# Optimization experiments

Hardware: AMD Instinct MI355X
Metric: run time of the kernel (lower is better)

## Reference

```python
import jax, jax.numpy as jnp
import numpy as np

B, IN_DIM, OUT_DIM, N = 8, 128, 128, 256
BN_EPS = 1e-5


def setup_inputs() -> dict:
    key = jax.random.key(0)
    ks = jax.random.split(key, 6)
    A = jax.random.normal(ks[0], (B, IN_DIM, N), dtype=jnp.float32)
    ini_p = float(np.sqrt(3.0 / OUT_DIM / IN_DIM))
    ini_qk = float(np.sqrt(1.0 / OUT_DIM / IN_DIM))
    P1 = jax.random.uniform(ks[1], (OUT_DIM, IN_DIM), minval=-ini_p, maxval=ini_p, dtype=jnp.float32)
    P2 = jax.random.uniform(ks[2], (OUT_DIM, IN_DIM), minval=-ini_p, maxval=ini_p, dtype=jnp.float32)
    q = jax.random.uniform(ks[3], (OUT_DIM, IN_DIM), minval=-ini_qk, maxval=ini_qk, dtype=jnp.float32)
    k = jax.random.uniform(ks[4], (OUT_DIM, IN_DIM), minval=-ini_qk, maxval=ini_qk, dtype=jnp.float32)
    gamma = jnp.ones((OUT_DIM,), dtype=jnp.float32)
    beta = jnp.zeros((OUT_DIM,), dtype=jnp.float32)
    return {"A": A, "P1": P1, "P2": P2, "q": q, "k": k,
            "gamma": gamma, "beta": beta,
            "permutation_size1": N, "BATCH_SIZE": B}


def reference(A, P1, P2, q, k, gamma, beta, permutation_size1, BATCH_SIZE):
    # A: [B, in_dim, n]; params [out_dim, in_dim]
    A1 = jnp.einsum('oi,bin->bon', P1, A)            # [B, C, n]
    Q = jnp.einsum('oi,bin->bon', q, A)              # [B, C, n]
    K = jnp.einsum('oi,bin->bon', k, A)              # [B, C, n]
    # Rank-1 outer product per (b, c): Alpha[b,c,i,j] = Q[b,c,i] * K[b,c,j]
    Alpha = Q[..., :, None] * K[..., None, :]        # [B, C, n, n]
    row_norm = jnp.linalg.norm(Alpha, axis=3, keepdims=True)  # [B, C, n, 1]
    Alpha_norm = jnp.abs(Alpha) / row_norm
    V = jnp.einsum('oi,bin->bon', P2, A)             # [B, C, n]
    Y = jnp.einsum('bcij,bcj->bci', Alpha_norm, V)   # [B, C, n]
    out = A1 + V + 0.1 * Y
    out = jax.nn.relu(out)
    # BatchNorm1d (training mode): normalize per channel over (B, n)
    mean = out.mean(axis=(0, 2), keepdims=True)
    var = out.var(axis=(0, 2), keepdims=True)
    out = (out - mean) * jax.lax.rsqrt(var + BN_EPS)
    out = out * gamma[None, :, None] + beta[None, :, None]
    return out
```

## Files before the change

### kernel.cpp

```cpp
#include <hip/hip_runtime.h>
#include <math.h>

#define BB   8
#define IND  128
#define OUTD 128
#define NN   256
#define NQ   64
#define BN_EPS 1e-5f

__global__ __launch_bounds__(64) void k1_proj(
    const float* __restrict__ A,
    const float* __restrict__ P1,
    const float* __restrict__ P2,
    const float* __restrict__ kw,
    float* __restrict__ pbuf,
    float* __restrict__ bnp)
{
    const int c = blockIdx.x;
    const int b = blockIdx.y;
    const int x = threadIdx.x;

    const float4* __restrict__ A4 = (const float4*)A + (size_t)b * IND * NQ;
    const float* __restrict__ w1 = P1 + c * IND;
    const float* __restrict__ w2 = P2 + c * IND;
    const float* __restrict__ w3 = kw + c * IND;

    float a1[4] = {0.f, 0.f, 0.f, 0.f};
    float vv[4] = {0.f, 0.f, 0.f, 0.f};
    float kv[4] = {0.f, 0.f, 0.f, 0.f};

    #pragma unroll
    for (int blk = 0; blk < 16; ++blk) {
        float4 cur[8];
        #pragma unroll
        for (int j = 0; j < 8; ++j)
            cur[j] = A4[(blk * 8 + j) * NQ + x];
        #pragma unroll
        for (int j = 0; j < 8; ++j) {
            const int i = blk * 8 + j;
            const float wa = w1[i], wb = w2[i], wc = w3[i];
            a1[0] = fmaf(wa, cur[j].x, a1[0]); a1[1] = fmaf(wa, cur[j].y, a1[1]);
            a1[2] = fmaf(wa, cur[j].z, a1[2]); a1[3] = fmaf(wa, cur[j].w, a1[3]);
            vv[0] = fmaf(wb, cur[j].x, vv[0]); vv[1] = fmaf(wb, cur[j].y, vv[1]);
            vv[2] = fmaf(wb, cur[j].z, vv[2]); vv[3] = fmaf(wb, cur[j].w, vv[3]);
            kv[0] = fmaf(wc, cur[j].x, kv[0]); kv[1] = fmaf(wc, cur[j].y, kv[1]);
            kv[2] = fmaf(wc, cur[j].z, kv[2]); kv[3] = fmaf(wc, cur[j].w, kv[3]);
        }
    }

    float s2 = 0.f, sv = 0.f;
    #pragma unroll
    for (int j = 0; j < 4; ++j) {
        s2 = fmaf(kv[j], kv[j], s2);
        sv = fmaf(fabsf(kv[j]), vv[j], sv);
    }
    #pragma unroll
    for (int off = 32; off >= 1; off >>= 1) {
        s2 += __shfl_xor(s2, off, 64);
        sv += __shfl_xor(sv, off, 64);
    }
    const float y = sv / sqrtf(s2);

    float p[4];
    float bnsum = 0.f, bnsq = 0.f;
    #pragma unroll
    for (int j = 0; j < 4; ++j) {
        float t = a1[j] + vv[j] + 0.1f * y;
        t = fmaxf(t, 0.f);
        p[j] = t;
        bnsum += t;
        bnsq  = fmaf(t, t, bnsq);
    }
    #pragma unroll
    for (int off = 32; off >= 1; off >>= 1) {
        bnsum += __shfl_xor(bnsum, off, 64);
        bnsq  += __shfl_xor(bnsq,  off, 64);
    }

    float4* __restrict__ p4 = (float4*)pbuf;
    p4[((size_t)b * OUTD + c) * NQ + x] = make_float4(p[0], p[1], p[2], p[3]);
    if (x == 0) {
        bnp[c * BB + b]              = bnsum;
        bnp[OUTD * BB + c * BB + b]  = bnsq;
    }
}

__global__ __launch_bounds__(512) void k2_bn(
    const float* __restrict__ pbuf,
    const float* __restrict__ bnp,
    const float* __restrict__ gamma,
    const float* __restrict__ beta,
    float* __restrict__ out)
{
    const int c = blockIdx.x;
    const int x = threadIdx.x;
    const int b = threadIdx.y;

    float tsum = 0.f, tsq = 0.f;
    #pragma unroll
    for (int w = 0; w < BB; ++w) {
        tsum += bnp[c * BB + w];
        tsq  += bnp[OUTD * BB + c * BB + w];
    }
    const float inv   = 1.f / (float)(BB * NN);
    const float mean  = tsum * inv;
    const float var   = tsq * inv - mean * mean;
    const float scale = gamma[c] * rsqrtf(var + BN_EPS);
    const float shift = beta[c] - mean * scale;

    const float4* __restrict__ p4 = (const float4*)pbuf;
    float4* __restrict__ out4 = (float4*)out;
    const size_t idx = ((size_t)b * OUTD + c) * NQ + x;
    const float4 p = p4[idx];
    out4[idx] = make_float4(fmaf(p.x, scale, shift), fmaf(p.y, scale, shift),
                            fmaf(p.z, scale, shift), fmaf(p.w, scale, shift));
}

extern "C" void kernel_launch(void* const* d_in, const int* in_sizes, int n_in,
                              void* d_out, int out_size, void* d_ws, size_t ws_size,
                              hipStream_t stream) {
    const float* A     = (const float*)d_in[0];
    const float* P1    = (const float*)d_in[1];
    const float* P2    = (const float*)d_in[2];
    const float* kw    = (const float*)d_in[4];
    const float* gamma = (const float*)d_in[5];
    const float* beta  = (const float*)d_in[6];
    float* out = (float*)d_out;

    float* pbuf = (float*)d_ws;
    float* bnp  = (float*)((char*)d_ws + (size_t)BB * OUTD * NN * sizeof(float));

    dim3 g1(OUTD, BB);
    k1_proj<<<g1, 64, 0, stream>>>(A, P1, P2, kw, pbuf, bnp);
    dim3 b2(64, BB);
    k2_bn<<<OUTD, b2, 0, stream>>>(pbuf, bnp, gamma, beta, out);
}
```

Before: 78.43 us.

## Fuse projection and batchnorm into one kernel with per-channel block reduction

Merges the projection kernel and the BatchNorm kernel into a single launch. Each block now handles one channel across all batches (64x8 threads), so the BN statistics are reduced through shared memory instead of a global workspace. This removes the intermediate pbuf round trip and one kernel launch. In exchange the grid shrinks from 1024 blocks of 64 threads to 128 blocks of 512 threads, which may lower parallelism across CUs.

```diff
diff --git a/kernel.cpp b/kernel.cpp
--- a/kernel.cpp
+++ b/kernel.cpp
@@ -8,16 +8,17 @@
 #define NQ   64
 #define BN_EPS 1e-5f
 
-__global__ __launch_bounds__(64) void k1_proj(
+__global__ __launch_bounds__(512) void k_fused(
     const float* __restrict__ A,
     const float* __restrict__ P1,
     const float* __restrict__ P2,
     const float* __restrict__ kw,
-    float* __restrict__ pbuf,
-    float* __restrict__ bnp)
+    const float* __restrict__ gamma,
+    const float* __restrict__ beta,
+    float* __restrict__ out)
 {
     const int c = blockIdx.x;
-    const int b = blockIdx.y;
+    const int b = threadIdx.y;
     const int x = threadIdx.x;
 
     const float4* __restrict__ A4 = (const float4*)A + (size_t)b * IND * NQ;
@@ -77,30 +78,18 @@
         bnsq  += __shfl_xor(bnsq,  off, 64);
     }
 
-    float4* __restrict__ p4 = (float4*)pbuf;
-    p4[((size_t)b * OUTD + c) * NQ + x] = make_float4(p[0], p[1], p[2], p[3]);
+    __shared__ float sred[2][BB];
     if (x == 0) {
-        bnp[c * BB + b]              = bnsum;
-        bnp[OUTD * BB + c * BB + b]  = bnsq;
+        sred[0][b] = bnsum;
+        sred[1][b] = bnsq;
     }
-}
-
-__global__ __launch_bounds__(512) void k2_bn(
-    const float* __restrict__ pbuf,
-    const float* __restrict__ bnp,
-    const float* __restrict__ gamma,
-    const float* __restrict__ beta,
-    float* __restrict__ out)
-{
-    const int c = blockIdx.x;
-    const int x = threadIdx.x;
-    const int b = threadIdx.y;
+    __syncthreads();
 
     float tsum = 0.f, tsq = 0.f;
     #pragma unroll
     for (int w = 0; w < BB; ++w) {
-        tsum += bnp[c * BB + w];
-        tsq  += bnp[OUTD * BB + c * BB + w];
+        tsum += sred[0][w];
+        tsq  += sred[1][w];
     }
     const float inv   = 1.f / (float)(BB * NN);
     const float mean  = tsum * inv;
@@ -108,12 +97,10 @@
     const float scale = gamma[c] * rsqrtf(var + BN_EPS);
     const float shift = beta[c] - mean * scale;
 
-    const float4* __restrict__ p4 = (const float4*)pbuf;
     float4* __restrict__ out4 = (float4*)out;
-    const size_t idx = ((size_t)b * OUTD + c) * NQ + x;
-    const float4 p = p4[idx];
-    out4[idx] = make_float4(fmaf(p.x, scale, shift), fmaf(p.y, scale, shift),
-                            fmaf(p.z, scale, shift), fmaf(p.w, scale, shift));
+    out4[((size_t)b * OUTD + c) * NQ + x] =
+        make_float4(fmaf(p[0], scale, shift), fmaf(p[1], scale, shift),
+                    fmaf(p[2], scale, shift), fmaf(p[3], scale, shift));
 }
 
 extern "C" void kernel_launch(void* const* d_in, const int* in_sizes, int n_in,
@@ -126,12 +113,8 @@
     const float* gamma = (const float*)d_in[5];
     const float* beta  = (const float*)d_in[6];
     float* out = (float*)d_out;
+    (void)d_ws; (void)ws_size;
 
-    float* pbuf = (float*)d_ws;
-    float* bnp  = (float*)((char*)d_ws + (size_t)BB * OUTD * NN * sizeof(float));
-
-    dim3 g1(OUTD, BB);
-    k1_proj<<<g1, 64, 0, stream>>>(A, P1, P2, kw, pbuf, bnp);
-    dim3 b2(64, BB);
-    k2_bn<<<OUTD, b2, 0, stream>>>(pbuf, bnp, gamma, beta, out);
+    dim3 blk(64, BB);
+    k_fused<<<OUTD, blk, 0, stream>>>(A, P1, P2, kw, gamma, beta, out);
 }
```

Result: no change. 79.88 us (+1.8%).
